# Kernel optimization log

Measured on AMD Instinct MI355X. Metric: run time of the kernel, lower is better.

## Reference

```python
import jax, jax.numpy as jnp
import numpy as np

NUM_SHOT = 1024
D_MODEL = 512
NHEAD = 8
NLAYERS = 6
D_FF = 2048
EPS = 1e-5


def _ln(x, s, b):
    m = jnp.mean(x, axis=-1, keepdims=True)
    v = jnp.mean(jnp.square(x - m), axis=-1, keepdims=True)
    return (x - m) / jnp.sqrt(v + EPS) * s + b


def _mha(q_in, kv_in, w_qkv, b_qkv, w_o, b_o):
    # q_in: [Sq, D], kv_in: [Sk, D]; PyTorch in_proj layout [3D, D]
    D = q_in.shape[-1]
    hd = D // NHEAD
    wq, wk, wv = w_qkv[:D], w_qkv[D:2 * D], w_qkv[2 * D:]
    bq, bk, bv = b_qkv[:D], b_qkv[D:2 * D], b_qkv[2 * D:]
    q = (q_in @ wq.T + bq).reshape(-1, NHEAD, hd)
    k = (kv_in @ wk.T + bk).reshape(-1, NHEAD, hd)
    v = (kv_in @ wv.T + bv).reshape(-1, NHEAD, hd)
    scores = jnp.einsum('qhd,khd->hqk', q, k) * (1.0 / np.sqrt(hd))
    a = jax.nn.softmax(scores, axis=-1)
    o = jnp.einsum('hqk,khd->qhd', a, v).reshape(-1, D)
    return o @ w_o.T + b_o


def setup_inputs() -> dict:
    key = jax.random.key(0)
    ks = iter(jax.random.split(key, 40))
    L, D, F = NLAYERS, D_MODEL, D_FF
    SC = 0.05  # weight scale, keeps activations sane

    def w(shape):
        return jax.random.normal(next(ks), shape, dtype=jnp.float32) * SC

    inp = {'shot_feature': jax.random.normal(next(ks), (NUM_SHOT, D), dtype=jnp.float32)}
    inp.update(
        enc_qkv_w=w((L, 3 * D, D)), enc_qkv_b=jnp.zeros((L, 3 * D), jnp.float32),
        enc_out_w=w((L, D, D)), enc_out_b=jnp.zeros((L, D), jnp.float32),
        enc_ff1_w=w((L, F, D)), enc_ff1_b=jnp.zeros((L, F), jnp.float32),
        enc_ff2_w=w((L, D, F)), enc_ff2_b=jnp.zeros((L, D), jnp.float32),
        enc_ln1_s=jnp.ones((L, D), jnp.float32), enc_ln1_b=jnp.zeros((L, D), jnp.float32),
        enc_ln2_s=jnp.ones((L, D), jnp.float32), enc_ln2_b=jnp.zeros((L, D), jnp.float32),
        dec_sa_qkv_w=w((L, 3 * D, D)), dec_sa_qkv_b=jnp.zeros((L, 3 * D), jnp.float32),
        dec_sa_out_w=w((L, D, D)), dec_sa_out_b=jnp.zeros((L, D), jnp.float32),
        dec_ca_qkv_w=w((L, 3 * D, D)), dec_ca_qkv_b=jnp.zeros((L, 3 * D), jnp.float32),
        dec_ca_out_w=w((L, D, D)), dec_ca_out_b=jnp.zeros((L, D), jnp.float32),
        dec_ff1_w=w((L, F, D)), dec_ff1_b=jnp.zeros((L, F), jnp.float32),
        dec_ff2_w=w((L, D, F)), dec_ff2_b=jnp.zeros((L, D), jnp.float32),
        dec_ln1_s=jnp.ones((L, D), jnp.float32), dec_ln1_b=jnp.zeros((L, D), jnp.float32),
        dec_ln2_s=jnp.ones((L, D), jnp.float32), dec_ln2_b=jnp.zeros((L, D), jnp.float32),
        dec_ln3_s=jnp.ones((L, D), jnp.float32), dec_ln3_b=jnp.zeros((L, D), jnp.float32),
        enc_norm_s=jnp.ones((D,), jnp.float32), enc_norm_b=jnp.zeros((D,), jnp.float32),
        dec_norm_s=jnp.ones((D,), jnp.float32), dec_norm_b=jnp.zeros((D,), jnp.float32),
    )
    return inp


def reference(shot_feature, enc_qkv_w, enc_qkv_b, enc_out_w, enc_out_b,
              enc_ff1_w, enc_ff1_b, enc_ff2_w, enc_ff2_b,
              enc_ln1_s, enc_ln1_b, enc_ln2_s, enc_ln2_b,
              dec_sa_qkv_w, dec_sa_qkv_b, dec_sa_out_w, dec_sa_out_b,
              dec_ca_qkv_w, dec_ca_qkv_b, dec_ca_out_w, dec_ca_out_b,
              dec_ff1_w, dec_ff1_b, dec_ff2_w, dec_ff2_b,
              dec_ln1_s, dec_ln1_b, dec_ln2_s, dec_ln2_b, dec_ln3_s, dec_ln3_b,
              enc_norm_s, enc_norm_b, dec_norm_s, dec_norm_b):
    x = shot_feature.reshape(NUM_SHOT, D_MODEL)  # batch dim of 1 squeezed

    # --- encoder (post-LN, ReLU FFN, dropout=eval identity) ---
    mem = x
    for i in range(NLAYERS):
        a = _mha(mem, mem, enc_qkv_w[i], enc_qkv_b[i], enc_out_w[i], enc_out_b[i])
        mem = _ln(mem + a, enc_ln1_s[i], enc_ln1_b[i])
        f = jax.nn.relu(mem @ enc_ff1_w[i].T + enc_ff1_b[i]) @ enc_ff2_w[i].T + enc_ff2_b[i]
        mem = _ln(mem + f, enc_ln2_s[i], enc_ln2_b[i])
    mem = _ln(mem, enc_norm_s, enc_norm_b)

    # --- decoder (tgt == src, no masks, matching original usage) ---
    y = x
    for i in range(NLAYERS):
        a = _mha(y, y, dec_sa_qkv_w[i], dec_sa_qkv_b[i], dec_sa_out_w[i], dec_sa_out_b[i])
        y = _ln(y + a, dec_ln1_s[i], dec_ln1_b[i])
        a = _mha(y, mem, dec_ca_qkv_w[i], dec_ca_qkv_b[i], dec_ca_out_w[i], dec_ca_out_b[i])
        y = _ln(y + a, dec_ln2_s[i], dec_ln2_b[i])
        f = jax.nn.relu(y @ dec_ff1_w[i].T + dec_ff1_b[i]) @ dec_ff2_w[i].T + dec_ff2_b[i]
        y = _ln(y + f, dec_ln3_s[i], dec_ln3_b[i])
    attention_out = _ln(y, dec_norm_s, dec_norm_b)  # [S, D]

    # --- fused pairwise cosine similarity (replaces O(n^2) python loop) ---
    n = attention_out / jnp.linalg.norm(attention_out, axis=1, keepdims=True)
    final_result = jax.lax.stop_gradient(n @ n.T)  # .detach() in original
    return (final_result, attention_out)
```

## Files before the change

### kernel.cpp

```cpp
#include <hip/hip_runtime.h>


#define NLAY 6

typedef __attribute__((ext_vector_type(8))) short short8;
typedef __attribute__((ext_vector_type(4))) short short4v;
typedef __attribute__((ext_vector_type(4))) float f32x4;

typedef __attribute__((address_space(3))) short lds_short;
typedef __attribute__((address_space(1))) const unsigned short g_ushort;

__device__ __forceinline__ void gload16(const unsigned short* g, short* l) {
    __builtin_amdgcn_global_load_lds((g_ushort*)g, (lds_short*)l, 16, 0, 0);
}

__device__ __forceinline__ void waitvm(int n) {
    if (n == 0)      asm volatile("s_waitcnt vmcnt(0)" ::: "memory");
    else if (n == 4) asm volatile("s_waitcnt vmcnt(4)" ::: "memory");
    else             asm volatile("s_waitcnt vmcnt(8)" ::: "memory");
}

__device__ inline unsigned short f2bu(float x) {
    unsigned u = __builtin_bit_cast(unsigned, x);
    unsigned r = (u + 0x7fffu + ((u >> 16) & 1u)) >> 16;
    return (unsigned short)r;
}

__device__ inline float b2f(unsigned short u) {
    return __builtin_bit_cast(float, (unsigned)u << 16);
}

struct WCvt {
    const float* src[10];
    unsigned short* dst[10];
    long cum[11];
};

__global__ __launch_bounds__(256)
void f2ball_k(WCvt wc)
{
    const long total = wc.cum[10];
    for (long c = (long)blockIdx.x * 256 + threadIdx.x; c < total;
         c += (long)gridDim.x * 256) {
        int t = 0;
        #pragma unroll
        for (int i = 1; i < 10; ++i) if (c >= wc.cum[i]) t = i;
        const long o = (c - wc.cum[t]) * 8;
        const float* s = wc.src[t];
        unsigned short* d = wc.dst[t];
        const float4 a = *(const float4*)(s + o);
        const float4 b = *(const float4*)(s + o + 4);
        short8 v;
        v[0] = (short)f2bu(a.x); v[1] = (short)f2bu(a.y);
        v[2] = (short)f2bu(a.z); v[3] = (short)f2bu(a.w);
        v[4] = (short)f2bu(b.x); v[5] = (short)f2bu(b.y);
        v[6] = (short)f2bu(b.z); v[7] = (short)f2bu(b.w);
        *(short8*)(d + o) = v;
    }
}

__global__ __launch_bounds__(256)
void f2b_k(const float* __restrict__ s, unsigned short* __restrict__ d, long n)
{
    const long stride = (long)gridDim.x * 256;
    for (long i = (long)blockIdx.x * 256 + threadIdx.x; i * 8 < n; i += stride) {
        const long o = i * 8;
        const float4 a = *(const float4*)(s + o);
        const float4 b = *(const float4*)(s + o + 4);
        short8 v;
        v[0] = (short)f2bu(a.x); v[1] = (short)f2bu(a.y);
        v[2] = (short)f2bu(a.z); v[3] = (short)f2bu(a.w);
        v[4] = (short)f2bu(b.x); v[5] = (short)f2bu(b.y);
        v[6] = (short)f2bu(b.z); v[7] = (short)f2bu(b.w);
        *(short8*)(d + o) = v;
    }
}

template<bool RELU, bool OBF16>
__global__ __launch_bounds__(256)
void gemm3_k(const unsigned short* __restrict__ A,
             const unsigned short* __restrict__ A2, int a2_col, int lda,
             const unsigned short* __restrict__ B, int ldb,
             const float* __restrict__ bias,
             void* __restrict__ Cv, int ldc, long sC,
             int K, float alpha,
             unsigned short* __restrict__ VTp, int vt_col0, int kz)
{
    __shared__ __align__(16) short As[3][4096];
    __shared__ __align__(16) short Bs[3][4096];
    const int bz = blockIdx.z;
    const int m0 = blockIdx.y * 64;
    const int n0 = blockIdx.x * 64;
    if (A2 && n0 >= a2_col) A = A2;
    A += (long)bz * kz;
    B += (long)bz * kz;
    const int tid = threadIdx.x;
    const int w  = tid >> 6;
    const int l  = tid & 63;
    const int fr = l & 15;
    const int kc = l >> 4;

    f32x4 acc[4] = {};
    const int T = K >> 6;

    auto FILL = [&](int t, int buf) {
        const int k0 = t * 64;
        #pragma unroll
        for (int it = 0; it < 2; ++it) {
            const int row = w * 16 + it * 8 + (l >> 3);
            const int sl  = ((l & 7) ^ (row & 7)) * 8;
            gload16(A + (long)(m0 + row) * lda + k0 + sl, &As[buf][(w * 16 + it * 8) * 64]);
            gload16(B + (long)(n0 + row) * ldb + k0 + sl, &Bs[buf][(w * 16 + it * 8) * 64]);
        }
    };

    FILL(0, 0);
    if (T > 1) FILL(1, 1);
    for (int t = 0; t < T; ++t) {
        waitvm(t + 1 < T ? 4 : 0);
        __builtin_amdgcn_sched_barrier(0);
        __builtin_amdgcn_s_barrier();
        if (t + 2 < T) FILL(t + 2, (t + 2) % 3);
        const int cb = t % 3;
        #pragma unroll
        for (int ks = 0; ks < 2; ++ks) {
            const int arow = w * 16 + fr;
            const short8 af = *(const short8*)&As[cb][arow * 64 + (((ks * 4 + kc) ^ (arow & 7)) * 8)];
            #pragma unroll
            for (int c = 0; c < 4; ++c) {
                const int brow = c * 16 + fr;
                const short8 bf = *(const short8*)&Bs[cb][brow * 64 + (((ks * 4 + kc) ^ (brow & 7)) * 8)];
                acc[c] = __builtin_amdgcn_mfma_f32_16x16x32_bf16(af, bf, acc[c], 0, 0, 0);
            }
        }
    }

    #pragma unroll
    for (int c = 0; c < 4; ++c) {
        const int n = n0 + c * 16 + fr;
        const float bv = bias ? bias[n] : 0.0f;
        const bool do_vt = (VTp != nullptr) && (n >= vt_col0);
        #pragma unroll
        for (int i = 0; i < 4; ++i) {
            const long m = m0 + w * 16 + kc * 4 + i;
            float v = acc[c][i] * alpha + bv;
            if (RELU) v = fmaxf(v, 0.0f);
            if (OBF16) ((unsigned short*)Cv)[bz * sC + m * ldc + n] = f2bu(v);
            else       ((float*)Cv)[bz * sC + m * ldc + n] = v;
            if (do_vt) {
                const int vc = n - vt_col0;
                VTp[(long)(vc >> 6) * 65536 + (long)(vc & 63) * 1024 + m] = f2bu(v);
            }
        }
    }
}

__global__ __launch_bounds__(128)
void attnp_k(const unsigned short* __restrict__ QKVb,
             const unsigned short* __restrict__ VT,
             const unsigned short* __restrict__ wo,
             unsigned short* __restrict__ SLABb)
{
    __shared__ __align__(16) short U[18432];
    short* Ks = U;
    short* Vs = U + 8192;
    short* Ps = U + 16384;
    const int qt = blockIdx.x;
    const int h  = blockIdx.y;
    const int tid = threadIdx.x;
    const int w  = tid >> 6;
    const int l  = tid & 63;
    const int fr = l & 15;
    const int kc = l >> 4;

    const int qrow = qt * 32 + w * 16 + fr;
    short8 qf[2];
    qf[0] = *(const short8*)(QKVb + (long)qrow * 1536 + h * 64 + kc * 8);
    qf[1] = *(const short8*)(QKVb + (long)qrow * 1536 + h * 64 + 32 + kc * 8);

    auto FILL = [&](int t, int buf) {
        const int kb = t * 64;
        #pragma unroll
        for (int it = 0; it < 4; ++it) {
            const int row = it * 16 + w * 8 + (l >> 3);
            const int sl  = ((l & 7) ^ (row & 7)) * 8;
            gload16(QKVb + (long)(kb + row) * 1536 + 512 + h * 64 + sl,
                    Ks + buf * 4096 + (it * 16 + w * 8) * 64);
            gload16(VT + (long)h * 65536 + (long)row * 1024 + kb + sl,
                    Vs + buf * 4096 + (it * 16 + w * 8) * 64);
        }
    };

    float m_i[4], l_i[4];
    f32x4 acc_o[4] = {};
    #pragma unroll
    for (int i = 0; i < 4; ++i) { m_i[i] = -1e30f; l_i[i] = 0.f; }

    short* ps = Ps + w * 1024;

    FILL(0, 0); FILL(1, 1);
    for (int t = 0; t < 16; ++t) {
        waitvm(t == 15 ? 0 : 8);
        __builtin_amdgcn_sched_barrier(0);
        __builtin_amdgcn_s_barrier();

        f32x4 sacc[4] = {};
        const int cb = t & 1;
        #pragma unroll
        for (int ks = 0; ks < 2; ++ks) {
            #pragma unroll
            for (int c = 0; c < 4; ++c) {
                const int krow = c * 16 + fr;
                const short8 kf = *(const short8*)(Ks + cb * 4096 + krow * 64 + (((ks * 4 + kc) ^ (krow & 7)) * 8));
                sacc[c] = __builtin_amdgcn_mfma_f32_16x16x32_bf16(qf[ks], kf, sacc[c], 0, 0, 0);
            }
        }

        float p[4][4];
        #pragma unroll
        for (int i = 0; i < 4; ++i) {
            float tm = fmaxf(fmaxf(sacc[0][i], sacc[1][i]), fmaxf(sacc[2][i], sacc[3][i]));
            #pragma unroll
            for (int off = 8; off; off >>= 1) tm = fmaxf(tm, __shfl_xor(tm, off));
            tm *= 0.125f;
            const float mn = fmaxf(m_i[i], tm);
            const float sc = __expf(m_i[i] - mn);
            m_i[i] = mn;
            float ts = 0.f;
            #pragma unroll
            for (int c = 0; c < 4; ++c) { p[c][i] = __expf(sacc[c][i] * 0.125f - mn); ts += p[c][i]; }
            #pragma unroll
            for (int off = 8; off; off >>= 1) ts += __shfl_xor(ts, off);
            l_i[i] = l_i[i] * sc + ts;
            #pragma unroll
            for (int c = 0; c < 4; ++c) acc_o[c][i] *= sc;
        }

        #pragma unroll
        for (int c = 0; c < 4; ++c) {
            const int col = c * 16 + fr;
            #pragma unroll
            for (int i = 0; i < 4; ++i) {
                const int row = kc * 4 + i;
                ps[row * 64 + (((col >> 3) ^ (row & 7)) * 8) + (col & 7)] = (short)f2bu(p[c][i]);
            }
        }
        short8 pf[2];
        pf[0] = *(const short8*)(ps + fr * 64 + ((kc ^ (fr & 7)) * 8));
        pf[1] = *(const short8*)(ps + fr * 64 + (((4 + kc) ^ (fr & 7)) * 8));

        #pragma unroll
        for (int ks = 0; ks < 2; ++ks) {
            #pragma unroll
            for (int c = 0; c < 4; ++c) {
                const int drow = c * 16 + fr;
                const short8 vf = *(const short8*)(Vs + cb * 4096 + drow * 64 + (((ks * 4 + kc) ^ (drow & 7)) * 8));
                acc_o[c] = __builtin_amdgcn_mfma_f32_16x16x32_bf16(pf[ks], vf, acc_o[c], 0, 0, 0);
            }
        }
        __builtin_amdgcn_s_barrier();
        if (t + 2 < 16) FILL(t + 2, (t + 2) & 1);
    }

    short* po = Ps + w * 1024;
    #pragma unroll
    for (int c = 0; c < 4; ++c) {
        const int col = c * 16 + fr;
        #pragma unroll
        for (int i = 0; i < 4; ++i) {
            const int r = kc * 4 + i;
            po[r * 64 + (((col >> 3) ^ (r & 7)) * 8) + (col & 7)] =
                (short)f2bu(acc_o[c][i] / l_i[i]);
        }
    }
    __syncthreads();

    short* Wos = U;
    unsigned short* SLABh = SLABb + (long)h * 524288;
    const int orow = qt * 32 + w * 16;

    auto WSTAGE = [&](int c8, int buf) {
        const int n0c = c8 * 64;
        #pragma unroll
        for (int it = 0; it < 4; ++it) {
            const int rb  = w * 32 + it * 8;
            const int row = rb + (l >> 3);
            const int sl  = ((l & 7) ^ (row & 7)) * 8;
            gload16(wo + (long)(n0c + row) * 512 + h * 64 + sl, Wos + buf * 4096 + rb * 64);
        }
    };

    WSTAGE(0, 0);
    for (int c8 = 0; c8 < 8; ++c8) {
        if (c8) __syncthreads();
        if (c8 + 1 < 8) WSTAGE(c8 + 1, (c8 + 1) & 1);
        waitvm(c8 + 1 < 8 ? 4 : 0);
        __builtin_amdgcn_sched_barrier(0);
        __builtin_amdgcn_s_barrier();
        const int buf = c8 & 1;
        f32x4 a2[4] = {};
        #pragma unroll
        for (int ks = 0; ks < 2; ++ks) {
            const int q = ks * 4 + kc;
            const short8 af = *(const short8*)(po + fr * 64 + ((q ^ (fr & 7)) * 8));
            #pragma unroll
            for (int ct = 0; ct < 4; ++ct) {
                const int brn = ct * 16 + fr;
                const short8 bf = *(const short8*)(Wos + buf * 4096 + brn * 64 + ((q ^ (brn & 7)) * 8));
                a2[ct] = __builtin_amdgcn_mfma_f32_16x16x32_bf16(af, bf, a2[ct], 0, 0, 0);
            }
        }
        #pragma unroll
        for (int ct = 0; ct < 4; ++ct) {
            const int n = c8 * 64 + ct * 16 + fr;
            #pragma unroll
            for (int i = 0; i < 4; ++i)
                SLABh[(long)(orow + kc * 4 + i) * 512 + n] = f2bu(a2[ct][i]);
        }
    }
}

template<int NSLAB, bool SB16>
__global__ __launch_bounds__(256)
void ln_k(const float* __restrict__ x, const void* __restrict__ slab,
          const float* __restrict__ bias,
          const float* __restrict__ s, const float* __restrict__ b,
          float* __restrict__ out, unsigned short* __restrict__ outb)
{
    const int lane = threadIdx.x & 63;
    const int row  = (blockIdx.x << 2) + (threadIdx.x >> 6);
    const float* px = x + (long)row * 512;
    float v[8];
    float sum = 0.f;
    #pragma unroll
    for (int i = 0; i < 8; ++i) {
        const int j = lane + (i << 6);
        v[i] = px[j];
        #pragma unroll
        for (int t = 0; t < NSLAB; ++t) {
            if (SB16) v[i] += b2f(((const unsigned short*)slab)[(long)t * 524288 + (long)row * 512 + j]);
            else      v[i] += ((const float*)slab)[(long)t * 524288 + (long)row * 512 + j];
        }
        if (NSLAB > 0) v[i] += bias[j];
        sum += v[i];
    }
    #pragma unroll
    for (int off = 32; off; off >>= 1) sum += __shfl_xor(sum, off);
    const float m = sum * (1.0f / 512.0f);
    float s2 = 0.f;
    #pragma unroll
    for (int i = 0; i < 8; ++i) { const float d = v[i] - m; s2 += d * d; }
    #pragma unroll
    for (int off = 32; off; off >>= 1) s2 += __shfl_xor(s2, off);
    const float inv = rsqrtf(s2 * (1.0f / 512.0f) + 1e-5f);
    #pragma unroll
    for (int i = 0; i < 8; ++i) {
        const int j = lane + (i << 6);
        const float r = (v[i] - m) * inv * s[j] + b[j];
        out[(long)row * 512 + j] = r;
        if (outb) outb[(long)row * 512 + j] = f2bu(r);
    }
}

__global__ __launch_bounds__(256)
void lnl2_k(const float* __restrict__ x,
            const float* __restrict__ s, const float* __restrict__ b,
            float* __restrict__ out_attn, unsigned short* __restrict__ nb)
{
    const int lane = threadIdx.x & 63;
    const int row  = (blockIdx.x << 2) + (threadIdx.x >> 6);
    const float* px = x + (long)row * 512;
    float v[8];
    float sum = 0.f;
    #pragma unroll
    for (int i = 0; i < 8; ++i) { v[i] = px[lane + (i << 6)]; sum += v[i]; }
    #pragma unroll
    for (int off = 32; off; off >>= 1) sum += __shfl_xor(sum, off);
    const float m = sum * (1.0f / 512.0f);
    float s2 = 0.f;
    #pragma unroll
    for (int i = 0; i < 8; ++i) { const float d = v[i] - m; s2 += d * d; }
    #pragma unroll
    for (int off = 32; off; off >>= 1) s2 += __shfl_xor(s2, off);
    const float inv = rsqrtf(s2 * (1.0f / 512.0f) + 1e-5f);
    float nrm = 0.f;
    #pragma unroll
    for (int i = 0; i < 8; ++i) {
        const int j = lane + (i << 6);
        v[i] = (v[i] - m) * inv * s[j] + b[j];
        out_attn[(long)row * 512 + j] = v[i];
        nrm += v[i] * v[i];
    }
    #pragma unroll
    for (int off = 32; off; off >>= 1) nrm += __shfl_xor(nrm, off);
    const float rinv = rsqrtf(nrm);
    #pragma unroll
    for (int i = 0; i < 8; ++i)
        nb[(long)row * 512 + lane + (i << 6)] = f2bu(v[i] * rinv);
}

__global__ __launch_bounds__(256)
void init_k(const float* __restrict__ x, float* __restrict__ mf, float* __restrict__ yf,
            unsigned short* __restrict__ mb, unsigned short* __restrict__ yb)
{
    const long i = ((long)blockIdx.x * 256 + threadIdx.x) * 4;
    const float4 v = *(const float4*)(x + i);
    *(float4*)(mf + i) = v;
    *(float4*)(yf + i) = v;
    short4v s;
    s[0] = (short)f2bu(v.x); s[1] = (short)f2bu(v.y);
    s[2] = (short)f2bu(v.z); s[3] = (short)f2bu(v.w);
    *(short4v*)(mb + i) = s;
    *(short4v*)(yb + i) = s;
}

static void gemm3(hipStream_t st, bool relu, bool obf16,
                  const unsigned short* A, int lda,
                  const unsigned short* B, int ldb,
                  const float* bias, void* C, int ldc, long sC,
                  int M, int N, int K, float alpha, int batch,
                  unsigned short* VTp = nullptr, int vt_col0 = 0,
                  const unsigned short* A2 = nullptr, int a2_col = 0,
                  int kz = 0)
{
    dim3 g(N / 64, M / 64, batch);
    if (obf16) {
        if (relu) gemm3_k<true,  true ><<<g, 256, 0, st>>>(A, A2, a2_col, lda, B, ldb, bias, C, ldc, sC, K, alpha, VTp, vt_col0, kz);
        else      gemm3_k<false, true ><<<g, 256, 0, st>>>(A, A2, a2_col, lda, B, ldb, bias, C, ldc, sC, K, alpha, VTp, vt_col0, kz);
    } else {
        if (relu) gemm3_k<true,  false><<<g, 256, 0, st>>>(A, A2, a2_col, lda, B, ldb, bias, C, ldc, sC, K, alpha, VTp, vt_col0, kz);
        else      gemm3_k<false, false><<<g, 256, 0, st>>>(A, A2, a2_col, lda, B, ldb, bias, C, ldc, sC, K, alpha, VTp, vt_col0, kz);
    }
}

extern "C" void kernel_launch(void* const* d_in, const int* in_sizes, int n_in,
                              void* d_out, int out_size, void* d_ws, size_t ws_size,
                              hipStream_t stream)
{
    const float* x            = (const float*)d_in[0];
    const float* enc_qkv_w    = (const float*)d_in[1];
    const float* enc_qkv_b    = (const float*)d_in[2];
    const float* enc_out_w    = (const float*)d_in[3];
    const float* enc_out_b    = (const float*)d_in[4];
    const float* enc_ff1_w    = (const float*)d_in[5];
    const float* enc_ff1_b    = (const float*)d_in[6];
    const float* enc_ff2_w    = (const float*)d_in[7];
    const float* enc_ff2_b    = (const float*)d_in[8];
    const float* enc_ln1_s    = (const float*)d_in[9];
    const float* enc_ln1_b    = (const float*)d_in[10];
    const float* enc_ln2_s    = (const float*)d_in[11];
    const float* enc_ln2_b    = (const float*)d_in[12];
    const float* dec_sa_qkv_w = (const float*)d_in[13];
    const float* dec_sa_qkv_b = (const float*)d_in[14];
    const float* dec_sa_out_w = (const float*)d_in[15];
    const float* dec_sa_out_b = (const float*)d_in[16];
    const float* dec_ca_qkv_w = (const float*)d_in[17];
    const float* dec_ca_qkv_b = (const float*)d_in[18];
    const float* dec_ca_out_w = (const float*)d_in[19];
    const float* dec_ca_out_b = (const float*)d_in[20];
    const float* dec_ff1_w    = (const float*)d_in[21];
    const float* dec_ff1_b    = (const float*)d_in[22];
    const float* dec_ff2_w    = (const float*)d_in[23];
    const float* dec_ff2_b    = (const float*)d_in[24];
    const float* dec_ln1_s    = (const float*)d_in[25];
    const float* dec_ln1_b    = (const float*)d_in[26];
    const float* dec_ln2_s    = (const float*)d_in[27];
    const float* dec_ln2_b    = (const float*)d_in[28];
    const float* dec_ln3_s    = (const float*)d_in[29];
    const float* dec_ln3_b    = (const float*)d_in[30];
    const float* enc_norm_s   = (const float*)d_in[31];
    const float* enc_norm_b   = (const float*)d_in[32];
    const float* dec_norm_s   = (const float*)d_in[33];
    const float* dec_norm_b   = (const float*)d_in[34];

    char* p = (char*)d_ws;
    auto alloc = [&](size_t bytes) -> char* {
        char* r = p; p += (bytes + 255) & ~(size_t)255; return r;
    };
    float*          MEMf = (float*)alloc(1024 * 512 * 4);
    float*          Yf   = (float*)alloc(1024 * 512 * 4);
    unsigned short* MEMb = (unsigned short*)alloc(1024 * 512 * 2);
    unsigned short* Yb   = (unsigned short*)alloc(1024 * 512 * 2);
    unsigned short* QKVb = (unsigned short*)alloc(1024 * 1536 * 2);
    unsigned short* VT   = (unsigned short*)alloc(8L * 64 * 1024 * 2);
    char*           SLAB = alloc(8L * 1024 * 512 * 2);
    unsigned short* F1b  = (unsigned short*)alloc(1024L * 2048 * 2);
    unsigned short* NBb  = (unsigned short*)alloc(1024 * 512 * 2);

    const float* wsrc[10] = {enc_qkv_w, enc_out_w, enc_ff1_w, enc_ff2_w,
                             dec_sa_qkv_w, dec_sa_out_w, dec_ca_qkv_w, dec_ca_out_w,
                             dec_ff1_w, dec_ff2_w};
    const long wper[10] = {1536L*512, 512L*512, 2048L*512, 512L*2048,
                           1536L*512, 512L*512, 1536L*512, 512L*512,
                           2048L*512, 512L*2048};
    long wtot = 0;
    for (int t = 0; t < 10; ++t) wtot += wper[t] * NLAY;

    const size_t used = (size_t)(p - (char*)d_ws);
    const bool preconv = (ws_size > used) && ((ws_size - used) >= (size_t)wtot * 2 + 4096);

    unsigned short* wpre[10] = {};
    unsigned short* slots[2] = {};
    int slot_ctr = 0;
    if (preconv) {
        WCvt wc;
        wc.cum[0] = 0;
        for (int t = 0; t < 10; ++t) {
            wpre[t] = (unsigned short*)alloc((size_t)wper[t] * NLAY * 2);
            wc.src[t] = wsrc[t];
            wc.dst[t] = wpre[t];
            wc.cum[t + 1] = wc.cum[t] + wper[t] * NLAY / 8;
        }
        f2ball_k<<<dim3(2048), 256, 0, stream>>>(wc);
    } else {
        slots[0] = (unsigned short*)alloc(2048L * 512 * 2);
        slots[1] = (unsigned short*)alloc(2048L * 512 * 2);
    }
    auto W = [&](int t, int layer) -> const unsigned short* {
        if (preconv) return wpre[t] + (long)layer * wper[t];
        unsigned short* dst = slots[(slot_ctr++) & 1];
        const long n = wper[t];
        long blocks = (n / 8 + 255) / 256; if (blocks > 2048) blocks = 2048;
        f2b_k<<<dim3((unsigned)blocks), 256, 0, stream>>>(wsrc[t] + (long)layer * wper[t], dst, n);
        return dst;
    };

    float* out_gram = (float*)d_out;
    float* out_attn = out_gram + 1024 * 1024;

    auto run_attn = [&](const unsigned short* qb, const unsigned short* kvb,
                        int wt_qkv, int wt_o, int layer, const float* bqkv,
                        const float* obias, const float* lns, const float* lnb,
                        float* xf, unsigned short* xb) {
        gemm3(stream, false, true, qb, 512, W(wt_qkv, layer), 512, bqkv,
              QKVb, 1536, 0, 1024, 1536, 512, 1.0f, 1, VT, 1024,
              (qb == kvb) ? nullptr : kvb, 512);
        attnp_k<<<dim3(32, 8), 128, 0, stream>>>(QKVb, VT, W(wt_o, layer),
                                                 (unsigned short*)SLAB);
        ln_k<8, true><<<256, 256, 0, stream>>>(xf, SLAB, obias, lns, lnb, xf, xb);
    };
    auto run_ffn = [&](unsigned short* inb, int wt1, int wt2, int layer,
                       const float* b1, const float* f2bias,
                       const float* lns, const float* lnb,
                       float* xf, unsigned short* xb) {
        gemm3(stream, true, true, inb, 512, W(wt1, layer), 512, b1,
              F1b, 2048, 0, 1024, 2048, 512, 1.0f, 1);
        gemm3(stream, false, false, F1b, 2048, W(wt2, layer), 2048, nullptr,
              SLAB, 512, 524288, 1024, 512, 512, 1.0f, 4, nullptr, 0, nullptr, 0, 512);
        ln_k<4, false><<<256, 256, 0, stream>>>(xf, SLAB, f2bias, lns, lnb, xf, xb);
    };

    init_k<<<512, 256, 0, stream>>>(x, MEMf, Yf, MEMb, Yb);

    for (int i = 0; i < NLAY; ++i) {
        run_attn(MEMb, MEMb, 0, 1, i, enc_qkv_b + i * 1536,
                 enc_out_b + i * 512, enc_ln1_s + i * 512, enc_ln1_b + i * 512, MEMf, MEMb);
        run_ffn(MEMb, 2, 3, i, enc_ff1_b + i * 2048, enc_ff2_b + i * 512,
                enc_ln2_s + i * 512, enc_ln2_b + i * 512, MEMf, MEMb);
    }
    ln_k<0, false><<<256, 256, 0, stream>>>(MEMf, nullptr, nullptr, enc_norm_s, enc_norm_b, MEMf, MEMb);

    for (int i = 0; i < NLAY; ++i) {
        run_attn(Yb, Yb, 4, 5, i, dec_sa_qkv_b + i * 1536,
                 dec_sa_out_b + i * 512, dec_ln1_s + i * 512, dec_ln1_b + i * 512, Yf, Yb);
        run_attn(Yb, MEMb, 6, 7, i, dec_ca_qkv_b + i * 1536,
                 dec_ca_out_b + i * 512, dec_ln2_s + i * 512, dec_ln2_b + i * 512, Yf, Yb);
        run_ffn(Yb, 8, 9, i, dec_ff1_b + i * 2048, dec_ff2_b + i * 512,
                dec_ln3_s + i * 512, dec_ln3_b + i * 512, Yf, Yb);
    }

    lnl2_k<<<256, 256, 0, stream>>>(Yf, dec_norm_s, dec_norm_b, out_attn, NBb);
    gemm3(stream, false, false, NBb, 512, NBb, 512, nullptr,
          out_gram, 1024, 0, 1024, 1024, 512, 1.0f, 1);
}
```

Measured before the change: 1.155 ms.

## Split attention keys across waves and batch cross-attention KV projections upfront

The attention kernel now gives each block 16 query rows and splits the 1024 keys between its two waves. Each wave runs its own online softmax with private double buffers and no per-tile barriers. The two partial results are merged through LDS, and the out-projection columns are split across the waves. Separately, the cross-attention K/V projections for all six decoder layers depend only on encoder memory, so they are computed in one batched GEMM after the encoder. Each decoder layer then only projects Q. This raises the grid size and removes serial launches, at the cost of more LDS per block and extra workspace.

```diff
diff --git a/kernel.cpp b/kernel.cpp
--- a/kernel.cpp
+++ b/kernel.cpp
@@ -15,9 +15,10 @@
 }
 
 __device__ __forceinline__ void waitvm(int n) {
-    if (n == 0)      asm volatile("s_waitcnt vmcnt(0)" ::: "memory");
-    else if (n == 4) asm volatile("s_waitcnt vmcnt(4)" ::: "memory");
-    else             asm volatile("s_waitcnt vmcnt(8)" ::: "memory");
+    if (n == 0)       asm volatile("s_waitcnt vmcnt(0)" ::: "memory");
+    else if (n == 4)  asm volatile("s_waitcnt vmcnt(4)" ::: "memory");
+    else if (n == 8)  asm volatile("s_waitcnt vmcnt(8)" ::: "memory");
+    else              asm volatile("s_waitcnt vmcnt(16)" ::: "memory");
 }
 
 __device__ inline unsigned short f2bu(float x) {
@@ -84,7 +85,8 @@
              const float* __restrict__ bias,
              void* __restrict__ Cv, int ldc, long sC,
              int K, float alpha,
-             unsigned short* __restrict__ VTp, int vt_col0, int kz)
+             unsigned short* __restrict__ VTp, int vt_col0, int kz,
+             long zB, int zBias, long zVT)
 {
     __shared__ __align__(16) short As[3][4096];
     __shared__ __align__(16) short Bs[3][4096];
@@ -93,7 +95,9 @@
     const int n0 = blockIdx.x * 64;
     if (A2 && n0 >= a2_col) A = A2;
     A += (long)bz * kz;
-    B += (long)bz * kz;
+    B += (long)bz * kz + (long)bz * zB;
+    if (bias) bias += (long)bz * zBias;
+    if (VTp)  VTp  += (long)bz * zVT;
     const int tid = threadIdx.x;
     const int w  = tid >> 6;
     const int l  = tid & 63;
@@ -156,15 +160,18 @@
 }
 
 __global__ __launch_bounds__(128)
-void attnp_k(const unsigned short* __restrict__ QKVb,
+void attnp_k(const unsigned short* __restrict__ Qb, int qld,
+             const unsigned short* __restrict__ Kb, int kld,
              const unsigned short* __restrict__ VT,
              const unsigned short* __restrict__ wo,
              unsigned short* __restrict__ SLABb)
 {
-    __shared__ __align__(16) short U[18432];
+    __shared__ __align__(16) short U[36928];
     short* Ks = U;
-    short* Vs = U + 8192;
-    short* Ps = U + 16384;
+    short* Vs = U + 16384;
+    short* Ps = U + 32768;
+    float* Of = (float*)(U + 34816);
+    float* Ml = (float*)(U + 34816 + 2048);
     const int qt = blockIdx.x;
     const int h  = blockIdx.y;
     const int tid = threadIdx.x;
@@ -173,21 +180,20 @@
     const int fr = l & 15;
     const int kc = l >> 4;
 
-    const int qrow = qt * 32 + w * 16 + fr;
+    const int qrow = qt * 16 + fr;
     short8 qf[2];
-    qf[0] = *(const short8*)(QKVb + (long)qrow * 1536 + h * 64 + kc * 8);
-    qf[1] = *(const short8*)(QKVb + (long)qrow * 1536 + h * 64 + 32 + kc * 8);
-
-    auto FILL = [&](int t, int buf) {
-        const int kb = t * 64;
-        #pragma unroll
-        for (int it = 0; it < 4; ++it) {
-            const int row = it * 16 + w * 8 + (l >> 3);
+    qf[0] = *(const short8*)(Qb + (long)qrow * qld + h * 64 + kc * 8);
+    qf[1] = *(const short8*)(Qb + (long)qrow * qld + h * 64 + 32 + kc * 8);
+
+    auto FILL = [&](int t, int lbuf) {
+        const int kb  = (w * 8 + t) * 64;
+        const int buf = w * 2 + lbuf;
+        #pragma unroll
+        for (int it = 0; it < 8; ++it) {
+            const int row = it * 8 + (l >> 3);
             const int sl  = ((l & 7) ^ (row & 7)) * 8;
-            gload16(QKVb + (long)(kb + row) * 1536 + 512 + h * 64 + sl,
-                    Ks + buf * 4096 + (it * 16 + w * 8) * 64);
-            gload16(VT + (long)h * 65536 + (long)row * 1024 + kb + sl,
-                    Vs + buf * 4096 + (it * 16 + w * 8) * 64);
+            gload16(Kb + (long)(kb + row) * kld + h * 64 + sl, Ks + buf * 4096 + it * 512);
+            gload16(VT + (long)h * 65536 + (long)row * 1024 + kb + sl, Vs + buf * 4096 + it * 512);
         }
     };
 
@@ -199,13 +205,12 @@
     short* ps = Ps + w * 1024;
 
     FILL(0, 0); FILL(1, 1);
-    for (int t = 0; t < 16; ++t) {
-        waitvm(t == 15 ? 0 : 8);
+    for (int t = 0; t < 8; ++t) {
+        waitvm(t == 7 ? 0 : 16);
         __builtin_amdgcn_sched_barrier(0);
-        __builtin_amdgcn_s_barrier();
+        const int cb = w * 2 + (t & 1);
 
         f32x4 sacc[4] = {};
-        const int cb = t & 1;
         #pragma unroll
         for (int ks = 0; ks < 2; ++ks) {
             #pragma unroll
@@ -258,46 +263,62 @@
                 acc_o[c] = __builtin_amdgcn_mfma_f32_16x16x32_bf16(pf[ks], vf, acc_o[c], 0, 0, 0);
             }
         }
-        __builtin_amdgcn_s_barrier();
-        if (t + 2 < 16) FILL(t + 2, (t + 2) & 1);
-    }
-
-    short* po = Ps + w * 1024;
-    #pragma unroll
-    for (int c = 0; c < 4; ++c) {
-        const int col = c * 16 + fr;
+        if (t + 2 < 8) FILL(t + 2, t & 1);
+    }
+
+    if (w == 1) {
+        #pragma unroll
+        for (int c = 0; c < 4; ++c)
+            #pragma unroll
+            for (int i = 0; i < 4; ++i)
+                Of[(kc * 4 + i) * 64 + c * 16 + fr] = acc_o[c][i];
+        if (fr == 0) {
+            #pragma unroll
+            for (int i = 0; i < 4; ++i) {
+                Ml[(kc * 4 + i) * 2]     = m_i[i];
+                Ml[(kc * 4 + i) * 2 + 1] = l_i[i];
+            }
+        }
+    }
+    __syncthreads();
+    short* po = Ps;
+    if (w == 0) {
         #pragma unroll
         for (int i = 0; i < 4; ++i) {
-            const int r = kc * 4 + i;
-            po[r * 64 + (((col >> 3) ^ (r & 7)) * 8) + (col & 7)] =
-                (short)f2bu(acc_o[c][i] / l_i[i]);
+            const int row = kc * 4 + i;
+            const float m1 = Ml[row * 2], l1 = Ml[row * 2 + 1];
+            const float M  = fmaxf(m_i[i], m1);
+            const float e0 = __expf(m_i[i] - M);
+            const float e1 = __expf(m1 - M);
+            const float inv = 1.0f / (e0 * l_i[i] + e1 * l1);
+            #pragma unroll
+            for (int c = 0; c < 4; ++c) {
+                const int col = c * 16 + fr;
+                const float o = e0 * acc_o[c][i] + e1 * Of[row * 64 + col];
+                po[row * 64 + (((col >> 3) ^ (row & 7)) * 8) + (col & 7)] = (short)f2bu(o * inv);
+            }
         }
     }
     __syncthreads();
 
-    short* Wos = U;
     unsigned short* SLABh = SLABb + (long)h * 524288;
-    const int orow = qt * 32 + w * 16;
-
-    auto WSTAGE = [&](int c8, int buf) {
+    auto WSTAGE = [&](int c8, int lbuf) {
         const int n0c = c8 * 64;
-        #pragma unroll
-        for (int it = 0; it < 4; ++it) {
-            const int rb  = w * 32 + it * 8;
-            const int row = rb + (l >> 3);
+        const int buf = w * 2 + lbuf;
+        #pragma unroll
+        for (int it = 0; it < 8; ++it) {
+            const int row = it * 8 + (l >> 3);
             const int sl  = ((l & 7) ^ (row & 7)) * 8;
-            gload16(wo + (long)(n0c + row) * 512 + h * 64 + sl, Wos + buf * 4096 + rb * 64);
+            gload16(wo + (long)(n0c + row) * 512 + h * 64 + sl, Ks + buf * 4096 + it * 512);
         }
     };
 
-    WSTAGE(0, 0);
-    for (int c8 = 0; c8 < 8; ++c8) {
-        if (c8) __syncthreads();
-        if (c8 + 1 < 8) WSTAGE(c8 + 1, (c8 + 1) & 1);
-        waitvm(c8 + 1 < 8 ? 4 : 0);
+    WSTAGE(w * 4, 0);
+    for (int j = 0; j < 4; ++j) {
+        if (j + 1 < 4) WSTAGE(w * 4 + j + 1, (j + 1) & 1);
+        waitvm(j + 1 < 4 ? 8 : 0);
         __builtin_amdgcn_sched_barrier(0);
-        __builtin_amdgcn_s_barrier();
-        const int buf = c8 & 1;
+        const int buf = w * 2 + (j & 1);
         f32x4 a2[4] = {};
         #pragma unroll
         for (int ks = 0; ks < 2; ++ks) {
@@ -306,16 +327,17 @@
             #pragma unroll
             for (int ct = 0; ct < 4; ++ct) {
                 const int brn = ct * 16 + fr;
-                const short8 bf = *(const short8*)(Wos + buf * 4096 + brn * 64 + ((q ^ (brn & 7)) * 8));
+                const short8 bf = *(const short8*)(Ks + buf * 4096 + brn * 64 + ((q ^ (brn & 7)) * 8));
                 a2[ct] = __builtin_amdgcn_mfma_f32_16x16x32_bf16(af, bf, a2[ct], 0, 0, 0);
             }
         }
+        const int c8 = w * 4 + j;
         #pragma unroll
         for (int ct = 0; ct < 4; ++ct) {
             const int n = c8 * 64 + ct * 16 + fr;
             #pragma unroll
             for (int i = 0; i < 4; ++i)
-                SLABh[(long)(orow + kc * 4 + i) * 512 + n] = f2bu(a2[ct][i]);
+                SLABh[(long)(qt * 16 + kc * 4 + i) * 512 + n] = f2bu(a2[ct][i]);
         }
     }
 }
@@ -421,15 +443,15 @@
                   int M, int N, int K, float alpha, int batch,
                   unsigned short* VTp = nullptr, int vt_col0 = 0,
                   const unsigned short* A2 = nullptr, int a2_col = 0,
-                  int kz = 0)
+                  int kz = 0, long zB = 0, int zBias = 0, long zVT = 0)
 {
     dim3 g(N / 64, M / 64, batch);
     if (obf16) {
-        if (relu) gemm3_k<true,  true ><<<g, 256, 0, st>>>(A, A2, a2_col, lda, B, ldb, bias, C, ldc, sC, K, alpha, VTp, vt_col0, kz);
-        else      gemm3_k<false, true ><<<g, 256, 0, st>>>(A, A2, a2_col, lda, B, ldb, bias, C, ldc, sC, K, alpha, VTp, vt_col0, kz);
+        if (relu) gemm3_k<true,  true ><<<g, 256, 0, st>>>(A, A2, a2_col, lda, B, ldb, bias, C, ldc, sC, K, alpha, VTp, vt_col0, kz, zB, zBias, zVT);
+        else      gemm3_k<false, true ><<<g, 256, 0, st>>>(A, A2, a2_col, lda, B, ldb, bias, C, ldc, sC, K, alpha, VTp, vt_col0, kz, zB, zBias, zVT);
     } else {
-        if (relu) gemm3_k<true,  false><<<g, 256, 0, st>>>(A, A2, a2_col, lda, B, ldb, bias, C, ldc, sC, K, alpha, VTp, vt_col0, kz);
-        else      gemm3_k<false, false><<<g, 256, 0, st>>>(A, A2, a2_col, lda, B, ldb, bias, C, ldc, sC, K, alpha, VTp, vt_col0, kz);
+        if (relu) gemm3_k<true,  false><<<g, 256, 0, st>>>(A, A2, a2_col, lda, B, ldb, bias, C, ldc, sC, K, alpha, VTp, vt_col0, kz, zB, zBias, zVT);
+        else      gemm3_k<false, false><<<g, 256, 0, st>>>(A, A2, a2_col, lda, B, ldb, bias, C, ldc, sC, K, alpha, VTp, vt_col0, kz, zB, zBias, zVT);
     }
 }
 
@@ -486,6 +508,9 @@
     char*           SLAB = alloc(8L * 1024 * 512 * 2);
     unsigned short* F1b  = (unsigned short*)alloc(1024L * 2048 * 2);
     unsigned short* NBb  = (unsigned short*)alloc(1024 * 512 * 2);
+    unsigned short* QB   = (unsigned short*)alloc(1024 * 512 * 2);
+    unsigned short* KVCA = (unsigned short*)alloc(6L * 1024 * 1024 * 2);
+    unsigned short* VTCA = (unsigned short*)alloc(6L * 8 * 64 * 1024 * 2);
 
     const float* wsrc[10] = {enc_qkv_w, enc_out_w, enc_ff1_w, enc_ff2_w,
                              dec_sa_qkv_w, dec_sa_out_w, dec_ca_qkv_w, dec_ca_out_w,
@@ -528,15 +553,14 @@
     float* out_gram = (float*)d_out;
     float* out_attn = out_gram + 1024 * 1024;
 
-    auto run_attn = [&](const unsigned short* qb, const unsigned short* kvb,
-                        int wt_qkv, int wt_o, int layer, const float* bqkv,
-                        const float* obias, const float* lns, const float* lnb,
+    auto run_self = [&](const unsigned short* xb_in, int wt_qkv, int wt_o, int layer,
+                        const float* bqkv, const float* obias,
+                        const float* lns, const float* lnb,
                         float* xf, unsigned short* xb) {
-        gemm3(stream, false, true, qb, 512, W(wt_qkv, layer), 512, bqkv,
-              QKVb, 1536, 0, 1024, 1536, 512, 1.0f, 1, VT, 1024,
-              (qb == kvb) ? nullptr : kvb, 512);
-        attnp_k<<<dim3(32, 8), 128, 0, stream>>>(QKVb, VT, W(wt_o, layer),
-                                                 (unsigned short*)SLAB);
+        gemm3(stream, false, true, xb_in, 512, W(wt_qkv, layer), 512, bqkv,
+              QKVb, 1536, 0, 1024, 1536, 512, 1.0f, 1, VT, 1024);
+        attnp_k<<<dim3(64, 8), 128, 0, stream>>>(QKVb, 1536, QKVb + 512, 1536, VT,
+                                                 W(wt_o, layer), (unsigned short*)SLAB);
         ln_k<8, true><<<256, 256, 0, stream>>>(xf, SLAB, obias, lns, lnb, xf, xb);
     };
     auto run_ffn = [&](unsigned short* inb, int wt1, int wt2, int layer,
@@ -553,18 +577,39 @@
     init_k<<<512, 256, 0, stream>>>(x, MEMf, Yf, MEMb, Yb);
 
     for (int i = 0; i < NLAY; ++i) {
-        run_attn(MEMb, MEMb, 0, 1, i, enc_qkv_b + i * 1536,
-                 enc_out_b + i * 512, enc_ln1_s + i * 512, enc_ln1_b + i * 512, MEMf, MEMb);
+        run_self(MEMb, 0, 1, i, enc_qkv_b + i * 1536, enc_out_b + i * 512,
+                 enc_ln1_s + i * 512, enc_ln1_b + i * 512, MEMf, MEMb);
         run_ffn(MEMb, 2, 3, i, enc_ff1_b + i * 2048, enc_ff2_b + i * 512,
                 enc_ln2_s + i * 512, enc_ln2_b + i * 512, MEMf, MEMb);
     }
     ln_k<0, false><<<256, 256, 0, stream>>>(MEMf, nullptr, nullptr, enc_norm_s, enc_norm_b, MEMf, MEMb);
 
+    if (preconv) {
+        gemm3(stream, false, true, MEMb, 512, wpre[6] + 512L * 512, 512,
+              dec_ca_qkv_b + 512, KVCA, 1024, 1024L * 1024,
+              1024, 1024, 512, 1.0f, 6, VTCA, 512,
+              nullptr, 0, 0, 1536L * 512, 1536, 524288L);
+    }
+
     for (int i = 0; i < NLAY; ++i) {
-        run_attn(Yb, Yb, 4, 5, i, dec_sa_qkv_b + i * 1536,
-                 dec_sa_out_b + i * 512, dec_ln1_s + i * 512, dec_ln1_b + i * 512, Yf, Yb);
-        run_attn(Yb, MEMb, 6, 7, i, dec_ca_qkv_b + i * 1536,
-                 dec_ca_out_b + i * 512, dec_ln2_s + i * 512, dec_ln2_b + i * 512, Yf, Yb);
+        run_self(Yb, 4, 5, i, dec_sa_qkv_b + i * 1536, dec_sa_out_b + i * 512,
+                 dec_ln1_s + i * 512, dec_ln1_b + i * 512, Yf, Yb);
+
+        if (preconv) {
+            gemm3(stream, false, true, Yb, 512, W(6, i), 512, dec_ca_qkv_b + i * 1536,
+                  QB, 512, 0, 1024, 512, 512, 1.0f, 1);
+            attnp_k<<<dim3(64, 8), 128, 0, stream>>>(QB, 512,
+                    KVCA + (long)i * 1024 * 1024, 1024, VTCA + (long)i * 524288,
+                    W(7, i), (unsigned short*)SLAB);
+        } else {
+            gemm3(stream, false, true, Yb, 512, W(6, i), 512, dec_ca_qkv_b + i * 1536,
+                  QKVb, 1536, 0, 1024, 1536, 512, 1.0f, 1, VT, 1024, MEMb, 512);
+            attnp_k<<<dim3(64, 8), 128, 0, stream>>>(QKVb, 1536, QKVb + 512, 1536, VT,
+                                                     W(7, i), (unsigned short*)SLAB);
+        }
+        ln_k<8, true><<<256, 256, 0, stream>>>(Yf, SLAB, dec_ca_out_b + i * 512,
+                                               dec_ln2_s + i * 512, dec_ln2_b + i * 512, Yf, Yb);
+
         run_ffn(Yb, 8, 9, i, dec_ff1_b + i * 2048, dec_ff2_b + i * 512,
                 dec_ln3_s + i * 512, dec_ln3_b + i * 512, Yf, Yb);
     }
```

Result: faster. 1.029 ms (-10.8%).
